# Kernel optimization log

Measured on AMD Instinct MI355X. Metric: run time of the kernel, lower is better.

The kernel has to match this reference:

```python
import jax, jax.numpy as jnp
import numpy as np

HEADS = 16
HEAD_DIM = 4  # attention_channels(64) // num_heads(16)


def setup_inputs() -> dict:
    key = jax.random.key(0)
    ks = jax.random.split(key, 9)
    C, AC = 256, 64
    N, H, W = 1, 64, 64
    s_in = 1.0 / np.sqrt(C)
    s_out = 1.0 / np.sqrt(AC)
    return {
        "X":  jax.random.normal(ks[0], (N, C, H, W), jnp.float32),
        "Wq": jax.random.normal(ks[1], (AC, C), jnp.float32) * s_in,
        "bq": jax.random.normal(ks[2], (AC,), jnp.float32) * 0.01,
        "Wk": jax.random.normal(ks[3], (AC, C), jnp.float32) * s_in,
        "bk": jax.random.normal(ks[4], (AC,), jnp.float32) * 0.01,
        "Wv": jax.random.normal(ks[5], (AC, C), jnp.float32) * s_in,
        "bv": jax.random.normal(ks[6], (AC,), jnp.float32) * 0.01,
        "Wo": jax.random.normal(ks[7], (C, AC), jnp.float32) * s_out,
        "bo": jax.random.normal(ks[8], (C,), jnp.float32) * 0.01,
    }


def _l2norm_over_dim(x, eps=1e-12):
    # torch F.normalize(dim=-2): x / max(||x||_2, eps) along head-dim axis
    n = jnp.sqrt(jnp.sum(x * x, axis=-2, keepdims=True))
    return x / jnp.maximum(n, eps)


def reference(X, Wq, bq, Wk, bk, Wv, bv, Wo, bo):
    N, C, H, W = X.shape
    L = H * W
    def proj(Wm, bm):
        # 1x1 conv == channel matmul; reshape to (N, heads, d, L)
        y = jnp.einsum('oc,nchw->nohw', Wm, X) + bm[None, :, None, None]
        return y.reshape(N, HEADS, HEAD_DIM, L)
    Q = _l2norm_over_dim(proj(Wq, bq))
    K = _l2norm_over_dim(proj(Wk, bk))
    V = proj(Wv, bv)
    # attention_weights[l, m] = q_l . k_m, softmax over m (rows)
    A = jax.nn.softmax(jnp.einsum('nhdl,nhdm->nhlm', Q, K), axis=-1)
    # faithful to original: out = V @ A  -> out[d, i] = sum_j V[d, j] * A[j, i]
    out = jnp.einsum('nhdj,nhji->nhdi', V, A)
    out = out.reshape(N, HEADS * HEAD_DIM, H, W)
    out = jnp.einsum('co,nohw->nchw', Wo, out) + bo[None, :, None, None]
    return out + X
```

## Files before the change

kernel.cpp:

```cpp
#include <hip/hip_runtime.h>
#include <math.h>


constexpr int SL = 4096;
constexpr int NF = 70;
constexpr int FP = 72;

__device__ __forceinline__ float invfact(int e) {
    return e < 2 ? 1.f : e == 2 ? 0.5f : e == 3 ? (1.f / 6.f) : (1.f / 24.f);
}
__device__ __forceinline__ float hdeg(int n) {
    return n == 0 ? 1.00004478f : n == 1 ? 0.99730766f
         : n == 2 ? 0.99839351f : n == 3 ? 1.06408440f : 1.05105416f;
}
__device__ __forceinline__ void f2abcd(int f, int& A, int& B, int& C, int& D) {
    for (int a = 0; a <= 4; ++a)
        for (int b = 0; b <= 4 - a; ++b)
            for (int c = 0; c <= 4 - a - b; ++c)
                for (int d = 0; d <= 4 - a - b - c; ++d)
                    if (f-- == 0) { A = a; B = b; C = c; D = d; return; }
}

#define FOR_MONOMIALS(BODY)                         \
    {                                               \
        int f = 0;                                  \
        _Pragma("unroll")                           \
        for (int a = 0; a <= 4; ++a)                \
        _Pragma("unroll")                           \
        for (int b = 0; b <= 4 - a; ++b)            \
        _Pragma("unroll")                           \
        for (int c = 0; c <= 4 - a - b; ++c)        \
        _Pragma("unroll")                           \
        for (int d = 0; d <= 4 - a - b - c; ++d) {  \
            BODY;                                   \
            ++f;                                    \
        }                                           \
    }

#define BUILD_POWERS(q)                                   \
    float p0[5], p1[5], p2[5], p3[5];                     \
    p0[0] = p1[0] = p2[0] = p3[0] = 1.f;                  \
    _Pragma("unroll")                                     \
    for (int t_ = 1; t_ < 5; ++t_) {                      \
        p0[t_] = p0[t_ - 1] * (q).x; p1[t_] = p1[t_ - 1] * (q).y; \
        p2[t_] = p2[t_ - 1] * (q).z; p3[t_] = p3[t_ - 1] * (q).w; }

__global__ __launch_bounds__(256) void qkv_kernel(
    const float* __restrict__ X,
    const float* __restrict__ Wq, const float* __restrict__ bq,
    const float* __restrict__ Wk, const float* __restrict__ bk,
    const float* __restrict__ Wv, const float* __restrict__ bv,
    float* __restrict__ Qn, float* __restrict__ Kn, float* __restrict__ V4)
{
    const int tid  = threadIdx.x;
    const int lane = tid & 63;
    const int wv   = __builtin_amdgcn_readfirstlane(tid >> 6);
    const int lt   = blockIdx.x;
    const int rb   = blockIdx.y;
    const int type = rb >> 2;
    const int rit  = (rb & 3) * 16 + wv * 4;
    const int l    = lt * 64 + lane;

    const float* W = type == 0 ? Wq : type == 1 ? Wk : Wv;
    const float* B = type == 0 ? bq : type == 1 ? bk : bv;
    const float* w0 = W + (rit + 0) * 256;
    const float* w1 = W + (rit + 1) * 256;
    const float* w2 = W + (rit + 2) * 256;
    const float* w3 = W + (rit + 3) * 256;

    float y0 = B[rit + 0], y1 = B[rit + 1], y2 = B[rit + 2], y3 = B[rit + 3];
    const float* Xl = X + l;
    #pragma unroll 8
    for (int c = 0; c < 256; ++c) {
        float x = Xl[c * SL];
        y0 = fmaf(w0[c], x, y0);
        y1 = fmaf(w1[c], x, y1);
        y2 = fmaf(w2[c], x, y2);
        y3 = fmaf(w3[c], x, y3);
    }
    if (type < 2) {
        float n = sqrtf(y0*y0 + y1*y1 + y2*y2 + y3*y3);
        float inv = 1.f / fmaxf(n, 1e-12f);
        y0 *= inv; y1 *= inv; y2 *= inv; y3 *= inv;
    }
    const int h = rit >> 2;
    float* base = type == 0 ? Qn : type == 1 ? Kn : V4;
    ((float4*)base)[h * SL + l] = make_float4(y0, y1, y2, y3);
}

template <int FC>
__device__ __forceinline__ void psi_accum(int h, int jc, int tid,
        const float* __restrict__ Kn, float acc[8])
{
    for (int u = 0; u < 4; ++u) {
        int j = jc * 1024 + u * 256 + tid;
        float4 k = ((const float4*)Kn)[h * SL + j];
        BUILD_POWERS(k)
        FOR_MONOMIALS({
            if (f >= FC * 8 && f < FC * 8 + 8)
                acc[f - FC * 8] += (p0[a] * p1[b]) * (p2[c] * p3[d]);
        })
    }
}

__global__ __launch_bounds__(256) void ssum_kernel(
    const float* __restrict__ Kn, float* __restrict__ Sp)
{
    const int tid = threadIdx.x;
    const int fc  = blockIdx.x;
    const int h   = blockIdx.y;
    const int jc  = blockIdx.z;
    float acc[8];
    #pragma unroll
    for (int k = 0; k < 8; ++k) acc[k] = 0.f;
    switch (fc) {
        case 0:  psi_accum<0>(h, jc, tid, Kn, acc); break;
        case 1:  psi_accum<1>(h, jc, tid, Kn, acc); break;
        case 2:  psi_accum<2>(h, jc, tid, Kn, acc); break;
        case 3:  psi_accum<3>(h, jc, tid, Kn, acc); break;
        case 4:  psi_accum<4>(h, jc, tid, Kn, acc); break;
        case 5:  psi_accum<5>(h, jc, tid, Kn, acc); break;
        case 6:  psi_accum<6>(h, jc, tid, Kn, acc); break;
        case 7:  psi_accum<7>(h, jc, tid, Kn, acc); break;
        default: psi_accum<8>(h, jc, tid, Kn, acc); break;
    }
    #pragma unroll
    for (int off = 32; off; off >>= 1)
        #pragma unroll
        for (int k = 0; k < 8; ++k) acc[k] += __shfl_down(acc[k], off);
    __shared__ float red[4][8];
    const int lane = tid & 63, wv = tid >> 6;
    if (lane == 0) {
        #pragma unroll
        for (int k = 0; k < 8; ++k) red[wv][k] = acc[k];
    }
    __syncthreads();
    if (tid < 8) {
        int f = fc * 8 + tid;
        if (f < NF) {
            float s = (red[0][tid] + red[1][tid]) + (red[2][tid] + red[3][tid]);
            int A, B, C, D; f2abcd(f, A, B, C, D);
            Sp[(jc * 16 + h) * FP + f] = s * hdeg(A + B + C + D) *
                ((invfact(A) * invfact(B)) * (invfact(C) * invfact(D)));
        }
    }
}

__global__ __launch_bounds__(256) void zvz_kernel(
    const float* __restrict__ Qn, const float* __restrict__ Sp,
    const float* __restrict__ V4, float* __restrict__ Vz)
{
    __shared__ float Sf[FP];
    const int tid = threadIdx.x;
    const int h   = blockIdx.y;
    if (tid < FP) {
        float s = 0.f;
        #pragma unroll
        for (int jc = 0; jc < 4; ++jc) s += Sp[(jc * 16 + h) * FP + tid];
        Sf[tid] = s;
    }
    __syncthreads();
    const int j = blockIdx.x * 256 + tid;
    float4 q = ((const float4*)Qn)[h * SL + j];
    BUILD_POWERS(q)
    float z = 0.f;
    FOR_MONOMIALS({ z = fmaf((p0[a]*p1[b])*(p2[c]*p3[d]), Sf[f], z); })
    float inv = 1.f / z;
    float4 v = ((const float4*)V4)[h * SL + j];
    ((float4*)Vz)[h * SL + j] = make_float4(v.x*inv, v.y*inv, v.z*inv, v.w*inv);
}

template <int FC>
__device__ __forceinline__ void m_accum(int h, int jc, int tid,
        const float* __restrict__ Qn, const float* __restrict__ Vz,
        float acc[32])
{
    for (int u = 0; u < 4; ++u) {
        int j = jc * 1024 + u * 256 + tid;
        float4 q = ((const float4*)Qn)[h * SL + j];
        float4 v = ((const float4*)Vz)[h * SL + j];
        BUILD_POWERS(q)
        FOR_MONOMIALS({
            if (f >= FC * 8 && f < FC * 8 + 8) {
                const int fi = f - FC * 8;
                float m = (p0[a] * p1[b]) * (p2[c] * p3[d]);
                acc[fi*4+0] = fmaf(m, v.x, acc[fi*4+0]);
                acc[fi*4+1] = fmaf(m, v.y, acc[fi*4+1]);
                acc[fi*4+2] = fmaf(m, v.z, acc[fi*4+2]);
                acc[fi*4+3] = fmaf(m, v.w, acc[fi*4+3]);
            }
        })
    }
}

__global__ __launch_bounds__(256) void mmat_kernel(
    const float* __restrict__ Qn, const float* __restrict__ Vz,
    float* __restrict__ Mp)
{
    const int tid = threadIdx.x;
    const int fc  = blockIdx.x;
    const int h   = blockIdx.y;
    const int jc  = blockIdx.z;
    float acc[32];
    #pragma unroll
    for (int k = 0; k < 32; ++k) acc[k] = 0.f;
    switch (fc) {
        case 0:  m_accum<0>(h, jc, tid, Qn, Vz, acc); break;
        case 1:  m_accum<1>(h, jc, tid, Qn, Vz, acc); break;
        case 2:  m_accum<2>(h, jc, tid, Qn, Vz, acc); break;
        case 3:  m_accum<3>(h, jc, tid, Qn, Vz, acc); break;
        case 4:  m_accum<4>(h, jc, tid, Qn, Vz, acc); break;
        case 5:  m_accum<5>(h, jc, tid, Qn, Vz, acc); break;
        case 6:  m_accum<6>(h, jc, tid, Qn, Vz, acc); break;
        case 7:  m_accum<7>(h, jc, tid, Qn, Vz, acc); break;
        default: m_accum<8>(h, jc, tid, Qn, Vz, acc); break;
    }
    #pragma unroll
    for (int off = 32; off; off >>= 1)
        #pragma unroll
        for (int k = 0; k < 32; ++k) acc[k] += __shfl_down(acc[k], off);
    __shared__ float red[4][32];
    const int lane = tid & 63, wv = tid >> 6;
    if (lane == 0) {
        #pragma unroll
        for (int k = 0; k < 32; ++k) red[wv][k] = acc[k];
    }
    __syncthreads();
    if (tid < 32) {
        int fi = tid >> 2, dd = tid & 3;
        int f = fc * 8 + fi;
        if (f < NF) {
            float s = (red[0][tid] + red[1][tid]) + (red[2][tid] + red[3][tid]);
            int A, B, C, D; f2abcd(f, A, B, C, D);
            s *= hdeg(A + B + C + D) *
                 (invfact(A) * invfact(B)) * (invfact(C) * invfact(D));
            Mp[((jc * 16 + h) * FP + f) * 4 + dd] = s;
        }
    }
}

__global__ __launch_bounds__(256) void outfuse_kernel(
    const float* __restrict__ Kn, const float* __restrict__ Mp,
    const float* __restrict__ Wo, const float* __restrict__ bo,
    const float* __restrict__ X, float* __restrict__ Y)
{
    __shared__ __align__(16) float ML[16 * FP * 4];
    __shared__ float AOL[64 * 33];
    const int tid = threadIdx.x;
    const int it  = blockIdx.x;
    const int cb  = blockIdx.y;
    const int i0  = it * 32;

    {
        const float4* Mp4 = (const float4*)Mp;
        float4* ML4 = (float4*)ML;
        #pragma unroll
        for (int w = 0; w < 5; ++w) {
            int e = tid + w * 256;
            if (e < 16 * FP) {
                float4 a = Mp4[e];
                float4 b = Mp4[16 * FP + e];
                float4 c = Mp4[32 * FP + e];
                float4 d = Mp4[48 * FP + e];
                ML4[e] = make_float4((a.x+b.x)+(c.x+d.x), (a.y+b.y)+(c.y+d.y),
                                     (a.z+b.z)+(c.z+d.z), (a.w+b.w)+(c.w+d.w));
            }
        }
    }
    __syncthreads();

    #pragma unroll
    for (int r = 0; r < 2; ++r) {
        int p = tid + r * 256;
        int pos = p & 31, h = p >> 5;
        float4 k = ((const float4*)Kn)[h * SL + i0 + pos];
        BUILD_POWERS(k)
        const float4* Mh = ((const float4*)ML) + h * FP;
        float a0 = 0.f, a1 = 0.f, a2 = 0.f, a3 = 0.f;
        FOR_MONOMIALS({
            float m = (p0[a] * p1[b]) * (p2[c] * p3[d]);
            float4 mm = Mh[f];
            a0 = fmaf(m, mm.x, a0); a1 = fmaf(m, mm.y, a1);
            a2 = fmaf(m, mm.z, a2); a3 = fmaf(m, mm.w, a3);
        })
        AOL[(h * 4 + 0) * 33 + pos] = a0;
        AOL[(h * 4 + 1) * 33 + pos] = a1;
        AOL[(h * 4 + 2) * 33 + pos] = a2;
        AOL[(h * 4 + 3) * 33 + pos] = a3;
    }
    __syncthreads();

    const int pos = tid & 31, cg = tid >> 5;
    const int chb = cb * 64 + cg * 8;
    float acc[8];
    #pragma unroll
    for (int u = 0; u < 8; ++u) acc[u] = 0.f;
    #pragma unroll 4
    for (int ob = 0; ob < 16; ++ob) {
        float x0 = AOL[(ob * 4 + 0) * 33 + pos];
        float x1 = AOL[(ob * 4 + 1) * 33 + pos];
        float x2 = AOL[(ob * 4 + 2) * 33 + pos];
        float x3 = AOL[(ob * 4 + 3) * 33 + pos];
        #pragma unroll
        for (int u = 0; u < 8; ++u) {
            float4 w4 = ((const float4*)Wo)[(chb + u) * 16 + ob];
            acc[u] = fmaf(w4.x, x0, fmaf(w4.y, x1,
                     fmaf(w4.z, x2, fmaf(w4.w, x3, acc[u]))));
        }
    }
    #pragma unroll
    for (int u = 0; u < 8; ++u) {
        int ch = chb + u;
        Y[ch * SL + i0 + pos] = acc[u] + bo[ch] + X[ch * SL + i0 + pos];
    }
}

extern "C" void kernel_launch(void* const* d_in, const int* in_sizes, int n_in,
                              void* d_out, int out_size, void* d_ws, size_t ws_size,
                              hipStream_t stream)
{
    const float* X  = (const float*)d_in[0];
    const float* Wq = (const float*)d_in[1];
    const float* bq = (const float*)d_in[2];
    const float* Wk = (const float*)d_in[3];
    const float* bk = (const float*)d_in[4];
    const float* Wv = (const float*)d_in[5];
    const float* bv = (const float*)d_in[6];
    const float* Wo = (const float*)d_in[7];
    const float* bo = (const float*)d_in[8];
    float* Y = (float*)d_out;

    char* w = (char*)d_ws;
    float* Qn = (float*)(w + (0 << 20));
    float* Kn = (float*)(w + (1 << 20));
    float* V4 = (float*)(w + (2 << 20));
    float* Vz = (float*)(w + (3 << 20));
    float* Sp = (float*)(w + (4 << 20));
    float* Mp = (float*)(w + (4 << 20) + (128 << 10));

    qkv_kernel<<<dim3(64, 12), 256, 0, stream>>>(X, Wq, bq, Wk, bk, Wv, bv,
                                                 Qn, Kn, V4);
    ssum_kernel<<<dim3(9, 16, 4), 256, 0, stream>>>(Kn, Sp);
    zvz_kernel<<<dim3(16, 16), 256, 0, stream>>>(Qn, Sp, V4, Vz);
    mmat_kernel<<<dim3(9, 16, 4), 256, 0, stream>>>(Qn, Vz, Mp);
    outfuse_kernel<<<dim3(128, 4), 256, 0, stream>>>(Kn, Mp, Wo, bo, X, Y);
}
```

Measured before the change: 119.6 us.

## Fuse key feature-sum into QKV projection and replace Vz with per-token inverse Z

Drops the separate ssum kernel. The K-projection waves now compute all 70 monomial features of each normalized key, reduce them across the wave with shuffles, and write per-tile partial sums; zvz then sums 64 partials per head and applies the scaling factors. zvz also stops writing a scaled V copy and stores only 1/z, which mmat applies on load. This saves one launch and some memory traffic, at the cost of roughly 70 live registers and many shuffles in the K-projection waves, which may hurt occupancy.

```diff
diff --git a/kernel.cpp b/kernel.cpp
--- a/kernel.cpp
+++ b/kernel.cpp
@@ -37,20 +37,21 @@
         }                                           \
     }
 
-#define BUILD_POWERS(q)                                   \
+#define BUILD_POWERS4(x0, x1, x2, x3)                     \
     float p0[5], p1[5], p2[5], p3[5];                     \
     p0[0] = p1[0] = p2[0] = p3[0] = 1.f;                  \
     _Pragma("unroll")                                     \
     for (int t_ = 1; t_ < 5; ++t_) {                      \
-        p0[t_] = p0[t_ - 1] * (q).x; p1[t_] = p1[t_ - 1] * (q).y; \
-        p2[t_] = p2[t_ - 1] * (q).z; p3[t_] = p3[t_ - 1] * (q).w; }
+        p0[t_] = p0[t_ - 1] * (x0); p1[t_] = p1[t_ - 1] * (x1); \
+        p2[t_] = p2[t_ - 1] * (x2); p3[t_] = p3[t_ - 1] * (x3); }
 
 __global__ __launch_bounds__(256) void qkv_kernel(
     const float* __restrict__ X,
     const float* __restrict__ Wq, const float* __restrict__ bq,
     const float* __restrict__ Wk, const float* __restrict__ bk,
     const float* __restrict__ Wv, const float* __restrict__ bv,
-    float* __restrict__ Qn, float* __restrict__ Kn, float* __restrict__ V4)
+    float* __restrict__ Qn, float* __restrict__ Kn, float* __restrict__ V4,
+    float* __restrict__ Sp)
 {
     const int tid  = threadIdx.x;
     const int lane = tid & 63;
@@ -86,100 +87,62 @@
     const int h = rit >> 2;
     float* base = type == 0 ? Qn : type == 1 ? Kn : V4;
     ((float4*)base)[h * SL + l] = make_float4(y0, y1, y2, y3);
-}
-
-template <int FC>
-__device__ __forceinline__ void psi_accum(int h, int jc, int tid,
-        const float* __restrict__ Kn, float acc[8])
-{
-    for (int u = 0; u < 4; ++u) {
-        int j = jc * 1024 + u * 256 + tid;
-        float4 k = ((const float4*)Kn)[h * SL + j];
-        BUILD_POWERS(k)
-        FOR_MONOMIALS({
-            if (f >= FC * 8 && f < FC * 8 + 8)
-                acc[f - FC * 8] += (p0[a] * p1[b]) * (p2[c] * p3[d]);
-        })
-    }
-}
-
-__global__ __launch_bounds__(256) void ssum_kernel(
-    const float* __restrict__ Kn, float* __restrict__ Sp)
-{
-    const int tid = threadIdx.x;
-    const int fc  = blockIdx.x;
-    const int h   = blockIdx.y;
-    const int jc  = blockIdx.z;
-    float acc[8];
-    #pragma unroll
-    for (int k = 0; k < 8; ++k) acc[k] = 0.f;
-    switch (fc) {
-        case 0:  psi_accum<0>(h, jc, tid, Kn, acc); break;
-        case 1:  psi_accum<1>(h, jc, tid, Kn, acc); break;
-        case 2:  psi_accum<2>(h, jc, tid, Kn, acc); break;
-        case 3:  psi_accum<3>(h, jc, tid, Kn, acc); break;
-        case 4:  psi_accum<4>(h, jc, tid, Kn, acc); break;
-        case 5:  psi_accum<5>(h, jc, tid, Kn, acc); break;
-        case 6:  psi_accum<6>(h, jc, tid, Kn, acc); break;
-        case 7:  psi_accum<7>(h, jc, tid, Kn, acc); break;
-        default: psi_accum<8>(h, jc, tid, Kn, acc); break;
-    }
-    #pragma unroll
-    for (int off = 32; off; off >>= 1)
-        #pragma unroll
-        for (int k = 0; k < 8; ++k) acc[k] += __shfl_down(acc[k], off);
-    __shared__ float red[4][8];
-    const int lane = tid & 63, wv = tid >> 6;
-    if (lane == 0) {
-        #pragma unroll
-        for (int k = 0; k < 8; ++k) red[wv][k] = acc[k];
-    }
-    __syncthreads();
-    if (tid < 8) {
-        int f = fc * 8 + tid;
-        if (f < NF) {
-            float s = (red[0][tid] + red[1][tid]) + (red[2][tid] + red[3][tid]);
-            int A, B, C, D; f2abcd(f, A, B, C, D);
-            Sp[(jc * 16 + h) * FP + f] = s * hdeg(A + B + C + D) *
-                ((invfact(A) * invfact(B)) * (invfact(C) * invfact(D)));
-        }
+
+    if (type == 1) {
+        BUILD_POWERS4(y0, y1, y2, y3)
+        float s[NF];
+        FOR_MONOMIALS({ s[f] = (p0[a] * p1[b]) * (p2[c] * p3[d]); })
+        #pragma unroll
+        for (int off = 32; off; off >>= 1)
+            #pragma unroll
+            for (int f = 0; f < NF; ++f) s[f] += __shfl_xor(s[f], off);
+        float* dst = Sp + (lt * 16 + h) * FP;
+        #pragma unroll
+        for (int f = 0; f < NF; ++f)
+            if (lane == (f & 63)) dst[f] = s[f];
     }
 }
 
 __global__ __launch_bounds__(256) void zvz_kernel(
     const float* __restrict__ Qn, const float* __restrict__ Sp,
-    const float* __restrict__ V4, float* __restrict__ Vz)
+    float* __restrict__ iZ)
 {
     __shared__ float Sf[FP];
     const int tid = threadIdx.x;
     const int h   = blockIdx.y;
     if (tid < FP) {
         float s = 0.f;
-        #pragma unroll
-        for (int jc = 0; jc < 4; ++jc) s += Sp[(jc * 16 + h) * FP + tid];
+        if (tid < NF) {
+            #pragma unroll 8
+            for (int lt = 0; lt < 64; ++lt)
+                s += Sp[(lt * 16 + h) * FP + tid];
+            int A, B, C, D; f2abcd(tid, A, B, C, D);
+            s *= hdeg(A + B + C + D) *
+                 ((invfact(A) * invfact(B)) * (invfact(C) * invfact(D)));
+        }
         Sf[tid] = s;
     }
     __syncthreads();
     const int j = blockIdx.x * 256 + tid;
     float4 q = ((const float4*)Qn)[h * SL + j];
-    BUILD_POWERS(q)
+    BUILD_POWERS4(q.x, q.y, q.z, q.w)
     float z = 0.f;
     FOR_MONOMIALS({ z = fmaf((p0[a]*p1[b])*(p2[c]*p3[d]), Sf[f], z); })
-    float inv = 1.f / z;
-    float4 v = ((const float4*)V4)[h * SL + j];
-    ((float4*)Vz)[h * SL + j] = make_float4(v.x*inv, v.y*inv, v.z*inv, v.w*inv);
+    iZ[h * SL + j] = 1.f / z;
 }
 
 template <int FC>
 __device__ __forceinline__ void m_accum(int h, int jc, int tid,
-        const float* __restrict__ Qn, const float* __restrict__ Vz,
-        float acc[32])
+        const float* __restrict__ Qn, const float* __restrict__ V4,
+        const float* __restrict__ iZ, float acc[32])
 {
     for (int u = 0; u < 4; ++u) {
         int j = jc * 1024 + u * 256 + tid;
         float4 q = ((const float4*)Qn)[h * SL + j];
-        float4 v = ((const float4*)Vz)[h * SL + j];
-        BUILD_POWERS(q)
+        float4 v = ((const float4*)V4)[h * SL + j];
+        float iz = iZ[h * SL + j];
+        v.x *= iz; v.y *= iz; v.z *= iz; v.w *= iz;
+        BUILD_POWERS4(q.x, q.y, q.z, q.w)
         FOR_MONOMIALS({
             if (f >= FC * 8 && f < FC * 8 + 8) {
                 const int fi = f - FC * 8;
@@ -194,8 +157,8 @@
 }
 
 __global__ __launch_bounds__(256) void mmat_kernel(
-    const float* __restrict__ Qn, const float* __restrict__ Vz,
-    float* __restrict__ Mp)
+    const float* __restrict__ Qn, const float* __restrict__ V4,
+    const float* __restrict__ iZ, float* __restrict__ Mp)
 {
     const int tid = threadIdx.x;
     const int fc  = blockIdx.x;
@@ -205,15 +168,15 @@
     #pragma unroll
     for (int k = 0; k < 32; ++k) acc[k] = 0.f;
     switch (fc) {
-        case 0:  m_accum<0>(h, jc, tid, Qn, Vz, acc); break;
-        case 1:  m_accum<1>(h, jc, tid, Qn, Vz, acc); break;
-        case 2:  m_accum<2>(h, jc, tid, Qn, Vz, acc); break;
-        case 3:  m_accum<3>(h, jc, tid, Qn, Vz, acc); break;
-        case 4:  m_accum<4>(h, jc, tid, Qn, Vz, acc); break;
-        case 5:  m_accum<5>(h, jc, tid, Qn, Vz, acc); break;
-        case 6:  m_accum<6>(h, jc, tid, Qn, Vz, acc); break;
-        case 7:  m_accum<7>(h, jc, tid, Qn, Vz, acc); break;
-        default: m_accum<8>(h, jc, tid, Qn, Vz, acc); break;
+        case 0:  m_accum<0>(h, jc, tid, Qn, V4, iZ, acc); break;
+        case 1:  m_accum<1>(h, jc, tid, Qn, V4, iZ, acc); break;
+        case 2:  m_accum<2>(h, jc, tid, Qn, V4, iZ, acc); break;
+        case 3:  m_accum<3>(h, jc, tid, Qn, V4, iZ, acc); break;
+        case 4:  m_accum<4>(h, jc, tid, Qn, V4, iZ, acc); break;
+        case 5:  m_accum<5>(h, jc, tid, Qn, V4, iZ, acc); break;
+        case 6:  m_accum<6>(h, jc, tid, Qn, V4, iZ, acc); break;
+        case 7:  m_accum<7>(h, jc, tid, Qn, V4, iZ, acc); break;
+        default: m_accum<8>(h, jc, tid, Qn, V4, iZ, acc); break;
     }
     #pragma unroll
     for (int off = 32; off; off >>= 1)
@@ -274,7 +237,7 @@
         int p = tid + r * 256;
         int pos = p & 31, h = p >> 5;
         float4 k = ((const float4*)Kn)[h * SL + i0 + pos];
-        BUILD_POWERS(k)
+        BUILD_POWERS4(k.x, k.y, k.z, k.w)
         const float4* Mh = ((const float4*)ML) + h * FP;
         float a0 = 0.f, a1 = 0.f, a2 = 0.f, a3 = 0.f;
         FOR_MONOMIALS({
@@ -334,14 +297,13 @@
     float* Qn = (float*)(w + (0 << 20));
     float* Kn = (float*)(w + (1 << 20));
     float* V4 = (float*)(w + (2 << 20));
-    float* Vz = (float*)(w + (3 << 20));
-    float* Sp = (float*)(w + (4 << 20));
-    float* Mp = (float*)(w + (4 << 20) + (128 << 10));
+    float* Sp = (float*)(w + (3 << 20));
+    float* iZ = (float*)(w + (3 << 20) + (512 << 10));
+    float* Mp = (float*)(w + (4 << 20));
 
     qkv_kernel<<<dim3(64, 12), 256, 0, stream>>>(X, Wq, bq, Wk, bk, Wv, bv,
-                                                 Qn, Kn, V4);
-    ssum_kernel<<<dim3(9, 16, 4), 256, 0, stream>>>(Kn, Sp);
-    zvz_kernel<<<dim3(16, 16), 256, 0, stream>>>(Qn, Sp, V4, Vz);
-    mmat_kernel<<<dim3(9, 16, 4), 256, 0, stream>>>(Qn, Vz, Mp);
+                                                 Qn, Kn, V4, Sp);
+    zvz_kernel<<<dim3(16, 16), 256, 0, stream>>>(Qn, Sp, iZ);
+    mmat_kernel<<<dim3(9, 16, 4), 256, 0, stream>>>(Qn, V4, iZ, Mp);
     outfuse_kernel<<<dim3(128, 4), 256, 0, stream>>>(Kn, Mp, Wo, bo, X, Y);
 }
```

Result: slower. 167.3 us (+39.9%).
